# Kernel optimization log

Measured on AMD Instinct MI355X. Metric: run time of the kernel, lower is better.

## Reference

```python
import jax, jax.numpy as jnp
import numpy as np

N_NODES = 100000
N_EDGES = 1600000
IN_FT = 128
OUT_FT = 32


def setup_inputs() -> dict:
    key = jax.random.key(0)
    k_seq, k_w, k_row, k_col, k_val = jax.random.split(key, 5)
    seq = jax.random.normal(k_seq, (N_NODES, IN_FT), dtype=jnp.float32)
    # xavier_uniform with gain=1.414 for weight [in_ft, out_ft]
    limit = 1.414 * np.sqrt(6.0 / (IN_FT + OUT_FT))
    weight = jax.random.uniform(k_w, (IN_FT, OUT_FT), dtype=jnp.float32,
                                minval=-limit, maxval=limit)
    edge_row = jax.random.randint(k_row, (N_EDGES,), 0, N_NODES, dtype=jnp.int64)
    edge_col = jax.random.randint(k_col, (N_EDGES,), 0, N_NODES, dtype=jnp.int64)
    edge_val = jax.random.uniform(k_val, (N_EDGES,), dtype=jnp.float32)
    return {"seq": seq, "weight": weight, "edge_row": edge_row,
            "edge_col": edge_col, "edge_val": edge_val}


def reference(seq, weight, edge_row, edge_col, edge_val):
    # support = seq @ weight : dense projection [N, out_ft]
    support = seq @ weight
    # out = spmm(adj, support): adj in COO (row, col, val), out[i] = sum_e val_e * support[col_e]
    msgs = edge_val[:, None] * support[edge_col]          # [E, out_ft]
    out = jax.ops.segment_sum(msgs, edge_row, num_segments=N_NODES)
    return jax.nn.relu(out)
```

## Files before the change

### kernel.cpp

```cpp
#include <hip/hip_runtime.h>
#include <hip/hip_bf16.h>
#include <hip/hip_fp16.h>

#define IN_FT  128
#define OUT_FT 32
#define APITCH 136

#define RPB   128
#define NBMAX 1024
#define CAP   4096
#define BA_T  1024
#define ACC_T 512
#define BIN_E 8192

typedef _Float16 f16x8 __attribute__((ext_vector_type(8)));
typedef __attribute__((ext_vector_type(4))) float f32x4;

union H2 { unsigned u; _Float16 h[2]; };

__global__ __launch_bounds__(256) void gcn_swz(const float* __restrict__ w,
                                               _Float16* __restrict__ wtab,
                                               int* __restrict__ bptr) {
    int t = threadIdx.x;
    bptr[t]       = 0;
    bptr[t + 256] = 0;
    bptr[t + 512] = 0;
    bptr[t + 768] = 0;
    for (int i = t; i < 2 * 4 * 64 * 8; i += 256) {
        int j    = i & 7;
        int lane = (i >> 3) & 63;
        int kt   = (i >> 9) & 3;
        int tile = i >> 11;
        int k    = kt * 32 + (lane >> 4) * 8 + j;
        int c    = (lane & 15) + tile * 16;
        wtab[i] = (_Float16)w[k * OUT_FT + c];
    }
}

__global__ __launch_bounds__(256) void gcn_gemm_mfma(const float* __restrict__ seq,
                                                     const _Float16* __restrict__ wtab,
                                                     unsigned short* __restrict__ sup,
                                                     int n) {
    __shared__ __align__(16) _Float16 at[64 * APITCH];
    const int t    = threadIdx.x;
    const int base = blockIdx.x * 64;

    for (int it = 0; it < 4; ++it) {
        int i     = it * 256 + t;
        int row_l = i >> 4;
        int c     = i & 15;
        int row   = base + row_l;
        f16x8 v = (f16x8)0;
        if (row < n) {
            const float4* p = (const float4*)(seq + (size_t)row * IN_FT + c * 8);
            float4 lo = p[0], hi = p[1];
            v[0] = (_Float16)lo.x; v[1] = (_Float16)lo.y;
            v[2] = (_Float16)lo.z; v[3] = (_Float16)lo.w;
            v[4] = (_Float16)hi.x; v[5] = (_Float16)hi.y;
            v[6] = (_Float16)hi.z; v[7] = (_Float16)hi.w;
        }
        *(f16x8*)&at[row_l * APITCH + c * 8] = v;
    }
    __syncthreads();

    const int wave = t >> 6;
    const int lane = t & 63;
    const int m    = lane & 15;
    const int quad = lane >> 4;

    const f16x8* wt = (const f16x8*)wtab;
    const int arow_l = wave * 16 + m;

    f32x4 acc0 = {0.f, 0.f, 0.f, 0.f};
    f32x4 acc1 = {0.f, 0.f, 0.f, 0.f};

    for (int kt = 0; kt < 4; ++kt) {
        f16x8 a  = *(const f16x8*)&at[arow_l * APITCH + kt * 32 + quad * 8];
        f16x8 b0 = wt[(0 * 4 + kt) * 64 + lane];
        f16x8 b1 = wt[(1 * 4 + kt) * 64 + lane];
        acc0 = __builtin_amdgcn_mfma_f32_16x16x32_f16(a, b0, acc0, 0, 0, 0);
        acc1 = __builtin_amdgcn_mfma_f32_16x16x32_f16(a, b1, acc1, 0, 0, 0);
    }

    for (int i = 0; i < 4; ++i) {
        int ro = base + wave * 16 + quad * 4 + i;
        if (ro < n) {
            _Float16 h0 = (_Float16)acc0[i];
            _Float16 h1 = (_Float16)acc1[i];
            sup[(size_t)ro * OUT_FT + m]      = *(unsigned short*)&h0;
            sup[(size_t)ro * OUT_FT + 16 + m] = *(unsigned short*)&h1;
        }
    }
}

__global__ __launch_bounds__(BA_T) void gcn_binA(const int* __restrict__ erow,
                                                 const int* __restrict__ ecol,
                                                 const float* __restrict__ eval,
                                                 int* __restrict__ bptr,
                                                 uint2* __restrict__ ebin, int nE) {
    __shared__ int cnt[NBMAX];
    __shared__ int cur[NBMAX];
    const int t  = threadIdx.x;
    const int cb = blockIdx.x * BIN_E;
    cnt[t] = 0;
    __syncthreads();

    int      rr[8];
    unsigned cq[8];

    #pragma unroll
    for (int k = 0; k < 2; ++k) {
        int i0 = cb + (k * BA_T + t) * 4;
        if (i0 + 4 <= nE) {
            int4   r4 = *(const int4*)&erow[i0];
            int4   c4 = *(const int4*)&ecol[i0];
            float4 v4 = *(const float4*)&eval[i0];
            rr[k * 4 + 0] = r4.x; rr[k * 4 + 1] = r4.y;
            rr[k * 4 + 2] = r4.z; rr[k * 4 + 3] = r4.w;
            cq[k * 4 + 0] = ((unsigned)c4.x << 15) | (unsigned)(v4.x * 32767.f + 0.5f);
            cq[k * 4 + 1] = ((unsigned)c4.y << 15) | (unsigned)(v4.y * 32767.f + 0.5f);
            cq[k * 4 + 2] = ((unsigned)c4.z << 15) | (unsigned)(v4.z * 32767.f + 0.5f);
            cq[k * 4 + 3] = ((unsigned)c4.w << 15) | (unsigned)(v4.w * 32767.f + 0.5f);
            atomicAdd(&cnt[r4.x >> 7], 1);
            atomicAdd(&cnt[r4.y >> 7], 1);
            atomicAdd(&cnt[r4.z >> 7], 1);
            atomicAdd(&cnt[r4.w >> 7], 1);
        } else {
            #pragma unroll
            for (int j = 0; j < 4; ++j) {
                int i = i0 + j;
                rr[k * 4 + j] = -1;
                if (i < nE) {
                    int r = erow[i];
                    rr[k * 4 + j] = r;
                    cq[k * 4 + j] = ((unsigned)ecol[i] << 15)
                                  | (unsigned)(eval[i] * 32767.f + 0.5f);
                    atomicAdd(&cnt[r >> 7], 1);
                }
            }
        }
    }
    __syncthreads();

    if (cnt[t]) cur[t] = atomicAdd(&bptr[t], cnt[t]);
    __syncthreads();

    #pragma unroll
    for (int k = 0; k < 8; ++k) {
        int r = rr[k];
        if (r >= 0) {
            int b = r >> 7;
            int p = atomicAdd(&cur[b], 1);
            if (p < CAP) {
                uint2 e;
                e.x = cq[k];
                e.y = (unsigned)(r & 127);
                ebin[(size_t)b * CAP + p] = e;
            }
        }
    }
}

__global__ __launch_bounds__(ACC_T) void gcn_acc(const uint2* __restrict__ ebin,
                                                 const int* __restrict__ bptr,
                                                 const unsigned* __restrict__ sup32,
                                                 float* __restrict__ out, int n) {
    __shared__ unsigned      cvS[CAP];
    __shared__ unsigned char ryS[CAP];
    __shared__ unsigned      csr[CAP];
    __shared__ int hist[RPB];
    __shared__ int segs[RPB];
    __shared__ int cursor[RPB];
    const int    t    = threadIdx.x;
    const int    b    = blockIdx.x;
    const int    cnt  = min(bptr[b], CAP);
    const size_t base = (size_t)b * CAP;

    if (t < RPB) hist[t] = 0;
    __syncthreads();

    for (int i = t; i < cnt; i += ACC_T) {
        uint2 e = ebin[base + i];
        cvS[i] = e.x;
        ryS[i] = (unsigned char)e.y;
        atomicAdd(&hist[e.y], 1);
    }
    __syncthreads();

    int v = 0;
    if (t < RPB) { v = hist[t]; segs[t] = v; }
    __syncthreads();
    for (int o = 1; o < RPB; o <<= 1) {
        int x = 0;
        if (t < RPB && t >= o) x = segs[t - o];
        __syncthreads();
        if (t < RPB) segs[t] += x;
        __syncthreads();
    }
    if (t < RPB) cursor[t] = segs[t] - v;
    __syncthreads();

    for (int i = t; i < cnt; i += ACC_T) {
        int p = atomicAdd(&cursor[ryS[i]], 1);
        csr[p] = cvS[i];
    }
    __syncthreads();

    const int g = t >> 3;
    const int j = t & 7;
    const int rbase = b * RPB;
    const uint2* sup2 = (const uint2*)sup32;
    for (int rr = g; rr < RPB; rr += ACC_T / 8) {
        int end = segs[rr];
        int st  = end - hist[rr];
        float a0 = 0.f, a1 = 0.f, a2 = 0.f, a3 = 0.f;
        int e = st;
        for (; e + 2 <= end; e += 2) {
            unsigned c0 = csr[e], c1 = csr[e + 1];
            uint2 s0 = sup2[(c0 >> 15) * 8 + j];
            uint2 s1 = sup2[(c1 >> 15) * 8 + j];
            float v0 = (float)(c0 & 0x7fffu) * (1.f / 32767.f);
            float v1 = (float)(c1 & 0x7fffu) * (1.f / 32767.f);
            H2 x0, y0, x1, y1;
            x0.u = s0.x; y0.u = s0.y; x1.u = s1.x; y1.u = s1.y;
            a0 += v0 * (float)x0.h[0] + v1 * (float)x1.h[0];
            a1 += v0 * (float)x0.h[1] + v1 * (float)x1.h[1];
            a2 += v0 * (float)y0.h[0] + v1 * (float)y1.h[0];
            a3 += v0 * (float)y0.h[1] + v1 * (float)y1.h[1];
        }
        if (e < end) {
            unsigned c0 = csr[e];
            uint2 s0 = sup2[(c0 >> 15) * 8 + j];
            float v0 = (float)(c0 & 0x7fffu) * (1.f / 32767.f);
            H2 x0, y0;
            x0.u = s0.x; y0.u = s0.y;
            a0 += v0 * (float)x0.h[0];
            a1 += v0 * (float)x0.h[1];
            a2 += v0 * (float)y0.h[0];
            a3 += v0 * (float)y0.h[1];
        }
        int row = rbase + rr;
        if (row < n) {
            float4 o;
            o.x = fmaxf(a0, 0.f);
            o.y = fmaxf(a1, 0.f);
            o.z = fmaxf(a2, 0.f);
            o.w = fmaxf(a3, 0.f);
            ((float4*)out)[(size_t)row * 8 + j] = o;
        }
    }
}

extern "C" void kernel_launch(void* const* d_in, const int* in_sizes, int n_in,
                              void* d_out, int out_size, void* d_ws, size_t ws_size,
                              hipStream_t stream) {
    const float* seq  = (const float*)d_in[0];
    const float* w    = (const float*)d_in[1];
    const int*   erow = (const int*)d_in[2];
    const int*   ecol = (const int*)d_in[3];
    const float* eval = (const float*)d_in[4];
    float* out = (float*)d_out;

    const int n_nodes = in_sizes[0] / IN_FT;
    const int n_edges = in_sizes[2];
    const int nB      = (n_nodes + RPB - 1) / RPB;

    unsigned short* sup  = (unsigned short*)d_ws;
    uint2*          ebin = (uint2*)(sup + (size_t)n_nodes * OUT_FT);
    int*            bptr = (int*)(ebin + (size_t)nB * CAP);
    _Float16*       wtab = (_Float16*)(bptr + NBMAX);

    gcn_swz<<<1, 256, 0, stream>>>(w, wtab, bptr);

    gcn_gemm_mfma<<<(n_nodes + 63) / 64, 256, 0, stream>>>(seq, wtab, sup, n_nodes);

    gcn_binA<<<(n_edges + BIN_E - 1) / BIN_E, BA_T, 0, stream>>>(erow, ecol, eval,
                                                                 bptr, ebin, n_edges);

    gcn_acc<<<nB, ACC_T, 0, stream>>>(ebin, bptr, (const unsigned*)sup,
                                      out, n_nodes);
}
```

Measured before the change: 146.1 us.

## Stage binned edges in LDS sorted by bucket before coalesced global write

The binning kernel now does a block-wide prefix scan over per-bucket counts, scatters each edge into shared memory grouped by bucket, and then has threads write consecutive slots to the global bins, finding each slot's bucket by binary search. This turns the scattered per-edge global stores into mostly contiguous runs per bucket, aimed at better write coalescing. In exchange it adds a 10-step scan with many barriers, about 40KB of extra LDS (which lowers occupancy), and a 10-step binary search per edge.

```diff
diff --git a/kernel.cpp b/kernel.cpp
--- a/kernel.cpp
+++ b/kernel.cpp
@@ -99,9 +99,15 @@
                                                  int* __restrict__ bptr,
                                                  uint2* __restrict__ ebin, int nE) {
     __shared__ int cnt[NBMAX];
-    __shared__ int cur[NBMAX];
-    const int t  = threadIdx.x;
-    const int cb = blockIdx.x * BIN_E;
+    __shared__ int lstart[NBMAX];
+    __shared__ int lcur[NBMAX];
+    __shared__ int gbase[NBMAX];
+    __shared__ unsigned      scv[BIN_E];
+    __shared__ unsigned char sry[BIN_E];
+    const int t   = threadIdx.x;
+    const int cb  = blockIdx.x * BIN_E;
+    const int ce  = min(cb + BIN_E, nE);
+    const int tot = ce - cb;
     cnt[t] = 0;
     __syncthreads();
 
@@ -142,7 +148,21 @@
     }
     __syncthreads();
 
-    if (cnt[t]) cur[t] = atomicAdd(&bptr[t], cnt[t]);
+    int v = cnt[t];
+    if (v) gbase[t] = atomicAdd(&bptr[t], v);
+
+    lstart[t] = v;
+    __syncthreads();
+    for (int o = 1; o < NBMAX; o <<= 1) {
+        int x = (t >= o) ? lstart[t - o] : 0;
+        __syncthreads();
+        lstart[t] += x;
+        __syncthreads();
+    }
+    int excl = lstart[t] - v;
+    __syncthreads();
+    lstart[t] = excl;
+    lcur[t]   = excl;
     __syncthreads();
 
     #pragma unroll
@@ -150,13 +170,26 @@
         int r = rr[k];
         if (r >= 0) {
             int b = r >> 7;
-            int p = atomicAdd(&cur[b], 1);
-            if (p < CAP) {
-                uint2 e;
-                e.x = cq[k];
-                e.y = (unsigned)(r & 127);
-                ebin[(size_t)b * CAP + p] = e;
-            }
+            int p = atomicAdd(&lcur[b], 1);
+            scv[p] = cq[k];
+            sry[p] = (unsigned char)(r & 127);
+        }
+    }
+    __syncthreads();
+
+    for (int i = t; i < tot; i += BA_T) {
+        int lo = 0, hi = NBMAX - 1;
+        #pragma unroll
+        for (int s = 0; s < 10; ++s) {
+            int mid = (lo + hi + 1) >> 1;
+            if (lstart[mid] <= i) lo = mid; else hi = mid - 1;
+        }
+        int off = gbase[lo] + (i - lstart[lo]);
+        if (off < CAP) {
+            uint2 e;
+            e.x = scv[i];
+            e.y = sry[i];
+            ebin[(size_t)lo * CAP + off] = e;
         }
     }
 }
```

After: 147.4 us. Within noise of the previous version (+0.9%).
